# Performance work log

Hardware: AMD Instinct MI355X
Metric: run time of the kernel (lower is better)

The kernel has to match this reference:

```python
import jax, jax.numpy as jnp
import numpy as np

GAMMA = 0.01
EPS = 0.01

def setup_inputs() -> dict:
    key = jax.random.key(0)
    k1, k2, k3 = jax.random.split(key, 3)
    B, T, IND, WIDTH = 512, 512, 64, 128
    x = jax.random.normal(k1, (B, T, IND), dtype=jnp.float32)
    init_state = jnp.zeros((1, B, WIDTH), dtype=jnp.float32)
    # xavier-uniform-like init for W and V
    lim_w = float(np.sqrt(6.0 / (WIDTH + WIDTH)))
    lim_v = float(np.sqrt(6.0 / (IND + WIDTH)))
    W = jax.random.uniform(k2, (WIDTH, WIDTH), jnp.float32, -lim_w, lim_w)
    V = jax.random.uniform(k3, (IND, WIDTH), jnp.float32, -lim_v, lim_v)
    b = jnp.zeros((WIDTH,), dtype=jnp.float32)
    return {"x": x, "init_state": init_state, "W": W, "V": V, "b": b}

def reference(x, init_state, W, V, b):
    # x: [B, T, ind]; init_state: [1, B, width]
    A = W - W.T  # antisymmetric matrix, computed once
    xV = jnp.einsum('bti,iw->btw', x, V) + b  # precompute input projection

    def step(state, u):
        # state: [B, width]; u: [B, width] (projected input at timestep t)
        new_state = state + EPS * jnp.tanh(state @ A - GAMMA * state + u)
        return new_state, new_state

    state0 = init_state[0]
    final_state, outputs = jax.lax.scan(step, state0, jnp.swapaxes(xV, 0, 1))
    outputs = jnp.swapaxes(outputs, 0, 1)  # [B, T, width]
    return outputs, final_state
```

## Files before the change

### kernel.cpp

```cpp
#include <hip/hip_runtime.h>
#include <hip/hip_bf16.h>

#define B_DIM 512
#define T_DIM 512
#define IND 64
#define WIDTH 128
#define GAMMA 0.01f
#define EPS 0.01f

#define PJ_ROWS 16
#define PJ_NT ((B_DIM * T_DIM) / PJ_ROWS)

__global__ __launch_bounds__(256) void proj_kernel(
    const float* __restrict__ x, const float* __restrict__ V,
    const float* __restrict__ bias, float* __restrict__ out) {
  __shared__ __align__(16) float xs[PJ_ROWS * IND];

  const int tid = threadIdx.x;
  const int c2 = (tid & 63) * 2;
  const int rh = tid >> 6;

  float2 Vreg[IND];
#pragma unroll
  for (int k = 0; k < IND; ++k)
    Vreg[k] = *(const float2*)(V + k * WIDTH + c2);
  const float2 bb = *(const float2*)(bias + c2);

  for (int tile = blockIdx.x; tile < PJ_NT; tile += gridDim.x) {
    const size_t m0 = (size_t)tile * PJ_ROWS;
    __syncthreads();
#pragma unroll
    for (int q = 0; q < 4; ++q)
      xs[tid + 256 * q] = x[m0 * IND + tid + 256 * q];
    __syncthreads();

    float2 acc0 = bb, acc1 = bb, acc2 = bb, acc3 = bb;
#pragma unroll
    for (int k4 = 0; k4 < IND / 4; ++k4) {
      float4 xv0 = ((const float4*)&xs[(rh + 0) * IND])[k4];
      float4 xv1 = ((const float4*)&xs[(rh + 4) * IND])[k4];
      float4 xv2 = ((const float4*)&xs[(rh + 8) * IND])[k4];
      float4 xv3 = ((const float4*)&xs[(rh + 12) * IND])[k4];
#pragma unroll
      for (int j = 0; j < 4; ++j) {
        float2 v = Vreg[4 * k4 + j];
        float e0 = (j == 0) ? xv0.x : (j == 1) ? xv0.y : (j == 2) ? xv0.z : xv0.w;
        float e1 = (j == 0) ? xv1.x : (j == 1) ? xv1.y : (j == 2) ? xv1.z : xv1.w;
        float e2 = (j == 0) ? xv2.x : (j == 1) ? xv2.y : (j == 2) ? xv2.z : xv2.w;
        float e3 = (j == 0) ? xv3.x : (j == 1) ? xv3.y : (j == 2) ? xv3.z : xv3.w;
        acc0.x += e0 * v.x; acc0.y += e0 * v.y;
        acc1.x += e1 * v.x; acc1.y += e1 * v.y;
        acc2.x += e2 * v.x; acc2.y += e2 * v.y;
        acc3.x += e3 * v.x; acc3.y += e3 * v.y;
      }
    }
    *(float2*)(out + (m0 + rh + 0) * WIDTH + c2) = acc0;
    *(float2*)(out + (m0 + rh + 4) * WIDTH + c2) = acc1;
    *(float2*)(out + (m0 + rh + 8) * WIDTH + c2) = acc2;
    *(float2*)(out + (m0 + rh + 12) * WIDTH + c2) = acc3;
  }
}

__global__ __launch_bounds__(512) void rnn_kernel(
    const float* __restrict__ W, const float* __restrict__ init,
    float* __restrict__ out, float* __restrict__ finals) {
  __shared__ __align__(16) float sL[2][WIDTH];
  const int b = blockIdx.x;
  const int tid = threadIdx.x;
  const int c = tid >> 2;
  const int kc = tid & 3;

  float Areg[32];
  {
    const int chunk = kc * 32;
#pragma unroll
    for (int j = 0; j < 8; ++j) {
      const int ri = (j + 2 * kc) & 7;
      const int k = chunk + ri * 4;
      float4 wr = *(const float4*)(W + (size_t)c * WIDTH + k);
      Areg[4 * j + 0] = W[(size_t)(k + 0) * WIDTH + c] - wr.x;
      Areg[4 * j + 1] = W[(size_t)(k + 1) * WIDTH + c] - wr.y;
      Areg[4 * j + 2] = W[(size_t)(k + 2) * WIDTH + c] - wr.z;
      Areg[4 * j + 3] = W[(size_t)(k + 3) * WIDTH + c] - wr.w;
    }
  }

  float s = init[(size_t)b * WIDTH + c];
  if (kc == 0) sL[0][c] = s;
  __syncthreads();

  float* outc = out + (size_t)b * T_DIM * WIDTH + c;
  float u0 = outc[0];
  float u1 = outc[WIDTH];

  const int base = kc * 8;
#pragma unroll 1
  for (int t = 0; t < T_DIM; ++t) {
    const int p = t & 1;
    const float u = u0;
    u0 = u1;
    if (t + 2 < T_DIM) u1 = outc[(size_t)(t + 2) * WIDTH];

    const float4* sp = (const float4*)&sL[p][0];
    float a0 = 0.f, a1 = 0.f, a2 = 0.f, a3 = 0.f;
#pragma unroll
    for (int j = 0; j < 8; ++j) {
      const int ri = (j + 2 * kc) & 7;
      float4 sv = sp[base + ri];
      a0 += sv.x * Areg[4 * j + 0];
      a1 += sv.y * Areg[4 * j + 1];
      a2 += sv.z * Areg[4 * j + 2];
      a3 += sv.w * Areg[4 * j + 3];
    }
    float dot = (a0 + a1) + (a2 + a3);
    dot += __shfl_xor(dot, 1);
    dot += __shfl_xor(dot, 2);

    const float f = dot - GAMMA * s + u;
    const float af = fabsf(f);
    const float e = __expf(-2.0f * af);
    float th = (1.0f - e) * __builtin_amdgcn_rcpf(1.0f + e);
    th = copysignf(th, f);
    const float ns = fmaf(EPS, th, s);

    if (kc == 0) {
      outc[(size_t)t * WIDTH] = ns;
      sL[p ^ 1][c] = ns;
    }
    s = ns;
    __syncthreads();
  }

  if (kc == 0) finals[(size_t)b * WIDTH + c] = s;
}

extern "C" void kernel_launch(void* const* d_in, const int* in_sizes, int n_in,
                              void* d_out, int out_size, void* d_ws,
                              size_t ws_size, hipStream_t stream) {
  const float* x = (const float*)d_in[0];
  const float* init = (const float*)d_in[1];
  const float* W = (const float*)d_in[2];
  const float* V = (const float*)d_in[3];
  const float* bias = (const float*)d_in[4];

  float* out = (float*)d_out;
  float* finals = out + (size_t)B_DIM * T_DIM * WIDTH;

  proj_kernel<<<2048, 256, 0, stream>>>(x, V, bias, out);
  rnn_kernel<<<B_DIM, 512, 0, stream>>>(W, init, out, finals);
}
```

Before: 328.0 us.

## Compute two state columns per thread in RNN kernel with DPP reductions

Each thread of the recurrent kernel now owns two output columns instead of one, so the block shrinks from 512 to 256 threads (four waves) and each shared-memory state load is reused for two dot products. The cross-lane reduction moves from __shfl_xor to DPP row moves, and tanh is computed as 1 - 2/(exp(2f)+1), which drops the abs and copysign. Fewer waves per block should make the per-step __syncthreads cheaper and cut LDS traffic, at the cost of twice as many weight registers per thread and less latency hiding. The new tanh form can overflow exp for large inputs, though rcp of infinity still gives the correct limit.

```diff
diff --git a/kernel.cpp b/kernel.cpp
--- a/kernel.cpp
+++ b/kernel.cpp
@@ -61,77 +61,96 @@
   }
 }
 
-__global__ __launch_bounds__(512) void rnn_kernel(
+template <int CTRL>
+__device__ __forceinline__ float dpp_mov(float x) {
+  return __int_as_float(
+      __builtin_amdgcn_update_dpp(0, __float_as_int(x), CTRL, 0xf, 0xf, true));
+}
+
+__global__ __launch_bounds__(256) void rnn_kernel(
     const float* __restrict__ W, const float* __restrict__ init,
     float* __restrict__ out, float* __restrict__ finals) {
   __shared__ __align__(16) float sL[2][WIDTH];
   const int b = blockIdx.x;
   const int tid = threadIdx.x;
-  const int c = tid >> 2;
   const int kc = tid & 3;
+  const int cp = tid >> 2;
+  const int c0 = 2 * cp;
 
-  float Areg[32];
+  float Areg[2][32];
   {
-    const int chunk = kc * 32;
+    const int k0 = kc * 32;
 #pragma unroll
     for (int j = 0; j < 8; ++j) {
       const int ri = (j + 2 * kc) & 7;
-      const int k = chunk + ri * 4;
-      float4 wr = *(const float4*)(W + (size_t)c * WIDTH + k);
-      Areg[4 * j + 0] = W[(size_t)(k + 0) * WIDTH + c] - wr.x;
-      Areg[4 * j + 1] = W[(size_t)(k + 1) * WIDTH + c] - wr.y;
-      Areg[4 * j + 2] = W[(size_t)(k + 2) * WIDTH + c] - wr.z;
-      Areg[4 * j + 3] = W[(size_t)(k + 3) * WIDTH + c] - wr.w;
+      const int k = k0 + ri * 4;
+#pragma unroll
+      for (int col = 0; col < 2; ++col) {
+        const int cc = c0 + col;
+        float4 wr = *(const float4*)(W + (size_t)cc * WIDTH + k);
+        Areg[col][4 * j + 0] = W[(size_t)(k + 0) * WIDTH + cc] - wr.x;
+        Areg[col][4 * j + 1] = W[(size_t)(k + 1) * WIDTH + cc] - wr.y;
+        Areg[col][4 * j + 2] = W[(size_t)(k + 2) * WIDTH + cc] - wr.z;
+        Areg[col][4 * j + 3] = W[(size_t)(k + 3) * WIDTH + cc] - wr.w;
+      }
     }
   }
 
-  float s = init[(size_t)b * WIDTH + c];
-  if (kc == 0) sL[0][c] = s;
+  float2 s = *(const float2*)(init + (size_t)b * WIDTH + c0);
+  if (kc == 0) *(float2*)&sL[0][c0] = s;
   __syncthreads();
 
-  float* outc = out + (size_t)b * T_DIM * WIDTH + c;
-  float u0 = outc[0];
-  float u1 = outc[WIDTH];
+  const float* uc = out + (size_t)b * T_DIM * WIDTH + c0;
+  float* outc = out + (size_t)b * T_DIM * WIDTH + c0;
+  float2 u0 = *(const float2*)(uc);
+  float2 u1 = *(const float2*)(uc + WIDTH);
 
-  const int base = kc * 8;
 #pragma unroll 1
   for (int t = 0; t < T_DIM; ++t) {
     const int p = t & 1;
-    const float u = u0;
+    const float2 u = u0;
     u0 = u1;
-    if (t + 2 < T_DIM) u1 = outc[(size_t)(t + 2) * WIDTH];
+    if (t + 2 < T_DIM) u1 = *(const float2*)(uc + (size_t)(t + 2) * WIDTH);
 
     const float4* sp = (const float4*)&sL[p][0];
-    float a0 = 0.f, a1 = 0.f, a2 = 0.f, a3 = 0.f;
+    float a00 = 0.f, a01 = 0.f, a10 = 0.f, a11 = 0.f;
 #pragma unroll
     for (int j = 0; j < 8; ++j) {
       const int ri = (j + 2 * kc) & 7;
-      float4 sv = sp[base + ri];
-      a0 += sv.x * Areg[4 * j + 0];
-      a1 += sv.y * Areg[4 * j + 1];
-      a2 += sv.z * Areg[4 * j + 2];
-      a3 += sv.w * Areg[4 * j + 3];
+      float4 sv = sp[kc * 8 + ri];
+      a00 += sv.x * Areg[0][4 * j + 0];
+      a01 += sv.y * Areg[0][4 * j + 1];
+      a00 += sv.z * Areg[0][4 * j + 2];
+      a01 += sv.w * Areg[0][4 * j + 3];
+      a10 += sv.x * Areg[1][4 * j + 0];
+      a11 += sv.y * Areg[1][4 * j + 1];
+      a10 += sv.z * Areg[1][4 * j + 2];
+      a11 += sv.w * Areg[1][4 * j + 3];
     }
-    float dot = (a0 + a1) + (a2 + a3);
-    dot += __shfl_xor(dot, 1);
-    dot += __shfl_xor(dot, 2);
+    float d0 = a00 + a01;
+    float d1 = a10 + a11;
+    d0 += dpp_mov<0xB1>(d0);
+    d1 += dpp_mov<0xB1>(d1);
+    d0 += dpp_mov<0x4E>(d0);
+    d1 += dpp_mov<0x4E>(d1);
 
-    const float f = dot - GAMMA * s + u;
-    const float af = fabsf(f);
-    const float e = __expf(-2.0f * af);
-    float th = (1.0f - e) * __builtin_amdgcn_rcpf(1.0f + e);
-    th = copysignf(th, f);
-    const float ns = fmaf(EPS, th, s);
+    const float f0 = d0 - GAMMA * s.x + u.x;
+    const float f1 = d1 - GAMMA * s.y + u.y;
+    const float e0 = __expf(2.0f * f0);
+    const float e1 = __expf(2.0f * f1);
+    const float th0 = fmaf(-2.0f, __builtin_amdgcn_rcpf(e0 + 1.0f), 1.0f);
+    const float th1 = fmaf(-2.0f, __builtin_amdgcn_rcpf(e1 + 1.0f), 1.0f);
+    s.x = fmaf(EPS, th0, s.x);
+    s.y = fmaf(EPS, th1, s.y);
 
     if (kc == 0) {
-      outc[(size_t)t * WIDTH] = ns;
-      sL[p ^ 1][c] = ns;
+      *(float2*)(outc + (size_t)t * WIDTH) = s;
+      *(float2*)&sL[p ^ 1][c0] = s;
     }
-    s = ns;
     __syncthreads();
   }
 
-  if (kc == 0) finals[(size_t)b * WIDTH + c] = s;
+  if (kc == 0) *(float2*)(finals + (size_t)b * WIDTH + c0) = s;
 }
 
 extern "C" void kernel_launch(void* const* d_in, const int* in_sizes, int n_in,
@@ -147,5 +166,5 @@
   float* finals = out + (size_t)B_DIM * T_DIM * WIDTH;
 
   proj_kernel<<<2048, 256, 0, stream>>>(x, V, bias, out);
-  rnn_kernel<<<B_DIM, 512, 0, stream>>>(W, init, out, finals);
+  rnn_kernel<<<B_DIM, 256, 0, stream>>>(W, init, out, finals);
 }
```

Result: faster. 301.8 us (-8.0%).
